# Kernel optimization log

Hardware: AMD Instinct MI355X
Metric: run time of the kernel (lower is better)

## Reference

```python
import jax, jax.numpy as jnp
import numpy as np


def setup_inputs() -> dict:
    key = jax.random.key(0)
    k1, k2, k3, k4 = jax.random.split(key, 4)
    H, D, Dh, NH = 4096, 1024, 256, 4  # height, weight1, INNER_FEATURE_A, heads
    x = jax.random.normal(k1, (H, D), dtype=jnp.float32)
    Wq = jax.random.normal(k2, (NH, D, Dh), dtype=jnp.float32)
    lin_w = jax.random.normal(k3, (D, NH * Dh), dtype=jnp.float32)  # torch Linear weight [out, in]
    lin_b = jax.random.normal(k4, (D,), dtype=jnp.float32)
    return {"x": x, "Wq": Wq, "lin_w": lin_w, "lin_b": lin_b}


def reference(x, Wq, lin_w, lin_b):
    # Faithful to source: Q = K = V = x @ Wq1 (original uses Wq1 for all three).
    # mask_flag=False -> multiplicative all-ones mask (identity, elided).
    # qkv: [heads, H, Dh]
    qkv = jnp.einsum('hd,ndk->nhk', x, Wq)
    # scores: [heads, H, H]; softmax over dim=1 of the 2D matrix = last axis here
    scores = jnp.einsum('nqk,npk->nqp', qkv, qkv)
    attn = jax.nn.softmax(scores, axis=-1)
    z = jnp.einsum('nqp,npk->nqk', attn, qkv)  # [heads, H, Dh]
    # concat heads along feature dim -> [H, heads*Dh]
    zc = jnp.transpose(z, (1, 0, 2)).reshape(x.shape[0], -1)
    return zc @ lin_w.T + lin_b
```

## Files before the change

### kernel.cpp

```cpp
#include <hip/hip_runtime.h>
#include <math.h>

#define SEQ 4096
#define DIM 1024
#define DHEAD 256
#define NHEADS 4

typedef __attribute__((ext_vector_type(8))) short bf16x8;
typedef __attribute__((ext_vector_type(4))) float f32x4;
typedef __attribute__((ext_vector_type(4))) short short4v;
typedef __attribute__((ext_vector_type(8))) short short8v;

__device__ __forceinline__ unsigned short f2b(float f) {
    union { float f; unsigned u; } v; v.f = f;
    unsigned r = v.u + 0x7FFFu + ((v.u >> 16) & 1u);
    return (unsigned short)(r >> 16);
}
__device__ __forceinline__ float b2f(unsigned short u) {
    union { unsigned u; float f; } v; v.u = ((unsigned)u) << 16;
    return v.f;
}

__device__ __forceinline__ void gll16(const void* g, void* lds) {
    __builtin_amdgcn_global_load_lds(
        (const __attribute__((address_space(1))) unsigned*)g,
        (__attribute__((address_space(3))) unsigned*)lds, 16, 0, 0);
}

__device__ __forceinline__ f32x4 mfma16(bf16x8 a, bf16x8 b, f32x4 c) {
    return __builtin_amdgcn_mfma_f32_16x16x32_bf16(a, b, c, 0, 0, 0);
}

__global__ __launch_bounds__(256)
void conv_kernel(const float* __restrict__ in, unsigned short* __restrict__ out, int n4) {
    int i = blockIdx.x * 256 + threadIdx.x;
    if (i >= n4) return;
    float4 v = ((const float4*)in)[i];
    short4v o;
    o[0] = (short)f2b(v.x); o[1] = (short)f2b(v.y);
    o[2] = (short)f2b(v.z); o[3] = (short)f2b(v.w);
    *(short4v*)(out + (size_t)i * 4) = o;
}

__global__ __launch_bounds__(256)
void wqt_kernel(const float* __restrict__ Wq, unsigned short* __restrict__ WqT) {
    __shared__ unsigned short T[64][72];
    const int tid = threadIdx.x;
    const int h = blockIdx.z;
    const int d0 = blockIdx.x * 64, c0 = blockIdx.y * 64;
#pragma unroll
    for (int it = 0; it < 4; ++it) {
        int f = tid + 256 * it;
        int row = f >> 4, cg = f & 15;
        float4 v = *(const float4*)&Wq[((size_t)(h * DIM + d0 + row)) * DHEAD + c0 + cg * 4];
        T[row][cg * 4 + 0] = f2b(v.x); T[row][cg * 4 + 1] = f2b(v.y);
        T[row][cg * 4 + 2] = f2b(v.z); T[row][cg * 4 + 3] = f2b(v.w);
    }
    __syncthreads();
#pragma unroll
    for (int it = 0; it < 2; ++it) {
        int f = tid + 256 * it;
        int cl = f >> 3, dg = f & 7;
        short8v o;
#pragma unroll
        for (int e = 0; e < 8; ++e) o[e] = (short)T[dg * 8 + e][cl];
        *(short8v*)&WqT[((size_t)(h * DHEAD + c0 + cl)) * DIM + d0 + dg * 8] = o;
    }
}

__global__ __launch_bounds__(256)
void qkvt_kernel(const unsigned short* __restrict__ qkv, unsigned short* __restrict__ qkvT) {
    __shared__ unsigned short T[64][72];
    const int tid = threadIdx.x;
    const int h = blockIdx.z;
    const int r0 = blockIdx.x * 64, c0 = blockIdx.y * 64;
#pragma unroll
    for (int it = 0; it < 2; ++it) {
        int f = tid + 256 * it;
        int row = f >> 3, cg = f & 7;
        short8v v = *(const short8v*)&qkv[((size_t)h * SEQ + r0 + row) * DHEAD + c0 + cg * 8];
#pragma unroll
        for (int e = 0; e < 8; ++e) T[row][cg * 8 + e] = (unsigned short)v[e];
    }
    __syncthreads();
#pragma unroll
    for (int it = 0; it < 2; ++it) {
        int f = tid + 256 * it;
        int cl = f >> 3, rg = f & 7;
        short8v o;
#pragma unroll
        for (int e = 0; e < 8; ++e) o[e] = (short)T[rg * 8 + e][cl];
        *(short8v*)&qkvT[((size_t)h * DHEAD + c0 + cl) * SEQ + r0 + rg * 8] = o;
    }
}

__global__ __launch_bounds__(256)
void qkv_gemm_kernel(const unsigned short* __restrict__ A,
                     const unsigned short* __restrict__ B,
                     unsigned short* __restrict__ qkv) {
    __shared__ unsigned short As[128 * 64];
    __shared__ unsigned short Bs[128 * 64];
    const int tid = threadIdx.x, w = tid >> 6, l = tid & 63;
    const int g = l >> 4, r16 = l & 15;
    const int m0 = blockIdx.x * 128, n0 = blockIdx.y * 128;
    const int wm = (w >> 1) * 64, wn = (w & 1) * 64;

    f32x4 acc[4][4];
#pragma unroll
    for (int mr = 0; mr < 4; ++mr)
#pragma unroll
        for (int nr = 0; nr < 4; ++nr) acc[mr][nr] = (f32x4){0.f, 0.f, 0.f, 0.f};

    for (int kb = 0; kb < DIM; kb += 64) {
        __syncthreads();
#pragma unroll
        for (int cc = 0; cc < 4; ++cc) {
            int row = w * 32 + cc * 8 + (l >> 3);
            int c = (l & 7) ^ (row & 7);
            gll16(&A[(size_t)(m0 + row) * DIM + kb + c * 8], &As[(size_t)(w * 32 + cc * 8) * 64]);
            gll16(&B[(size_t)(n0 + row) * DIM + kb + c * 8], &Bs[(size_t)(w * 32 + cc * 8) * 64]);
        }
        __syncthreads();
#pragma unroll
        for (int s = 0; s < 2; ++s) {
            bf16x8 af[4], bf[4];
#pragma unroll
            for (int mr = 0; mr < 4; ++mr) {
                int row = wm + mr * 16 + r16;
                int st = (s * 4 + g) ^ (row & 7);
                af[mr] = *(const bf16x8*)&As[row * 64 + st * 8];
            }
#pragma unroll
            for (int nr = 0; nr < 4; ++nr) {
                int row = wn + nr * 16 + r16;
                int st = (s * 4 + g) ^ (row & 7);
                bf[nr] = *(const bf16x8*)&Bs[row * 64 + st * 8];
            }
#pragma unroll
            for (int mr = 0; mr < 4; ++mr)
#pragma unroll
                for (int nr = 0; nr < 4; ++nr)
                    acc[mr][nr] = mfma16(af[mr], bf[nr], acc[mr][nr]);
        }
    }
#pragma unroll
    for (int mr = 0; mr < 4; ++mr)
#pragma unroll
        for (int nr = 0; nr < 4; ++nr) {
            int n = n0 + wn + nr * 16 + r16;
            int h = n >> 8, c = n & 255;
#pragma unroll
            for (int r = 0; r < 4; ++r) {
                int m = m0 + wm + mr * 16 + g * 4 + r;
                qkv[((size_t)h * SEQ + m) * DHEAD + c] = f2b(acc[mr][nr][r]);
            }
        }
}

__global__ __launch_bounds__(256, 2)
void attn_kernel(const unsigned short* __restrict__ qkv,
                 const unsigned short* __restrict__ qkvT,
                 unsigned short* __restrict__ p0,
                 unsigned short* __restrict__ p1,
                 float* __restrict__ ml) {
    __shared__ unsigned short Ks[64 * 256];
    __shared__ unsigned short Vt[256 * 64];
    __shared__ unsigned short Ps[64 * 64];
    __shared__ float alphaS[64];
    __shared__ float mS[64], lS[64];

    const int tid = threadIdx.x, w = tid >> 6, l = tid & 63;
    const int g = l >> 4, r16 = l & 15;
    const int bid = blockIdx.x;
    const int h = (bid & 7) >> 1, hf = bid & 1;
    const int qb = bid >> 3;
    const unsigned short* __restrict__ qh = qkv + (size_t)h * SEQ * DHEAD;
    const unsigned short* __restrict__ qth = qkvT + (size_t)h * DHEAD * SEQ;
    const int jb0 = hf * (SEQ / 2);
    const int NT = (SEQ / 2) / 64;

    bf16x8 qf[8];
    {
        const unsigned short* qrow = qh + (size_t)(qb * 64 + w * 16 + r16) * DHEAD + g * 8;
#pragma unroll
        for (int s = 0; s < 8; ++s) qf[s] = *(const bf16x8*)(qrow + s * 32);
    }

    f32x4 Oacc[16];
#pragma unroll
    for (int i = 0; i < 16; ++i) Oacc[i] = (f32x4){0.f, 0.f, 0.f, 0.f};
    float mrow = -INFINITY, lrow = 0.f;

    for (int t = 0; t < NT; ++t) {
        const int jb = jb0 + t * 64;
        __syncthreads();
#pragma unroll
        for (int cc = 0; cc < 8; ++cc) {
            int ch = w * 8 + cc;
            int j = ch * 2 + (l >> 5);
            int cp = l & 31;
            int c = (cp & 24) | ((cp & 7) ^ (j & 7));
            gll16(&qh[(size_t)(jb + j) * DHEAD + c * 8], &Ks[(size_t)ch * 512]);
        }
#pragma unroll
        for (int cc = 0; cc < 8; ++cc) {
            int ch = w * 8 + cc;
            int d = ch * 8 + (l >> 3);
            int c = (l & 7) ^ (d & 7);
            gll16(&qth[(size_t)d * SEQ + jb + c * 8], &Vt[(size_t)ch * 512]);
        }
        __syncthreads();

        f32x4 sacc[4];
#pragma unroll
        for (int jt = 0; jt < 4; ++jt) sacc[jt] = (f32x4){0.f, 0.f, 0.f, 0.f};
        __builtin_amdgcn_s_setprio(1);
#pragma unroll
        for (int s = 0; s < 8; ++s)
#pragma unroll
            for (int jt = 0; jt < 4; ++jt) {
                int j = jt * 16 + r16;
                int c = s * 4 + g;
                int st = (c & 24) | ((c & 7) ^ (j & 7));
                bf16x8 af = *(const bf16x8*)&Ks[j * 256 + st * 8];
                sacc[jt] = mfma16(af, qf[s], sacc[jt]);
            }
        __builtin_amdgcn_s_setprio(0);

        float mx = sacc[0][0];
#pragma unroll
        for (int jt = 0; jt < 4; ++jt)
#pragma unroll
            for (int r = 0; r < 4; ++r) mx = fmaxf(mx, sacc[jt][r]);
        mx = fmaxf(mx, __shfl_xor(mx, 16, 64));
        mx = fmaxf(mx, __shfl_xor(mx, 32, 64));

        float mn = fmaxf(mrow, mx);
        float alpha = __expf(mrow - mn);
        mrow = mn;

        float rsum = 0.f;
        short4v pf[4];
#pragma unroll
        for (int jt = 0; jt < 4; ++jt)
#pragma unroll
            for (int r = 0; r < 4; ++r) {
                float p = __expf(sacc[jt][r] - mrow);
                rsum += p;
                pf[jt][r] = (short)f2b(p);
            }
        rsum += __shfl_xor(rsum, 16, 64);
        rsum += __shfl_xor(rsum, 32, 64);
        lrow = lrow * alpha + rsum;

#pragma unroll
        for (int jt = 0; jt < 4; ++jt) {
            int st = (jt * 2 + (g >> 1)) ^ (r16 & 7);
            *(short4v*)&Ps[(w * 16 + r16) * 64 + st * 8 + (g & 1) * 4] = pf[jt];
        }
        if (g == 0) alphaS[w * 16 + r16] = alpha;
        __syncthreads();

        bf16x8 pa[8];
#pragma unroll
        for (int qs = 0; qs < 4; ++qs) {
            f32x4 av = *(const f32x4*)&alphaS[qs * 16 + g * 4];
#pragma unroll
            for (int dt = 0; dt < 4; ++dt)
#pragma unroll
                for (int r = 0; r < 4; ++r) Oacc[qs * 4 + dt][r] *= av[r];
#pragma unroll
            for (int s2 = 0; s2 < 2; ++s2) {
                int qrow = qs * 16 + r16;
                int st = (s2 * 4 + g) ^ (qrow & 7);
                pa[qs * 2 + s2] = *(const bf16x8*)&Ps[qrow * 64 + st * 8];
            }
        }
        __builtin_amdgcn_s_setprio(1);
#pragma unroll
        for (int dt = 0; dt < 4; ++dt) {
            int d = w * 64 + dt * 16 + r16;
#pragma unroll
            for (int s2 = 0; s2 < 2; ++s2) {
                int st = (s2 * 4 + g) ^ (d & 7);
                bf16x8 bv = *(const bf16x8*)&Vt[d * 64 + st * 8];
#pragma unroll
                for (int qs = 0; qs < 4; ++qs)
                    Oacc[qs * 4 + dt] = mfma16(pa[qs * 2 + s2], bv, Oacc[qs * 4 + dt]);
            }
        }
        __builtin_amdgcn_s_setprio(0);
    }

    if (g == 0) { mS[w * 16 + r16] = mrow; lS[w * 16 + r16] = lrow; }
    __syncthreads();
    unsigned short* po = hf ? p1 : p0;
#pragma unroll
    for (int qs = 0; qs < 4; ++qs)
#pragma unroll
        for (int dt = 0; dt < 4; ++dt) {
            int d = w * 64 + dt * 16 + r16;
#pragma unroll
            for (int r = 0; r < 4; ++r) {
                int q = qb * 64 + qs * 16 + g * 4 + r;
                po[(size_t)q * (NHEADS * DHEAD) + h * DHEAD + d] = f2b(Oacc[qs * 4 + dt][r]);
            }
        }
    if (tid < 64) {
        int q = qb * 64 + tid;
        float* mlq = ml + ((size_t)(hf * NHEADS + h) * SEQ + q) * 2;
        mlq[0] = mS[tid]; mlq[1] = lS[tid];
    }
}

__global__ __launch_bounds__(256)
void combine_kernel(const unsigned short* __restrict__ pa,
                    const unsigned short* __restrict__ pb,
                    const float* __restrict__ ml,
                    unsigned short* __restrict__ zc) {
    size_t t = (size_t)blockIdx.x * 256 + threadIdx.x;
    size_t f = t * 8;
    int q = (int)(f >> 10);
    int h = (int)((f >> 8) & 3);
    const float* ml0 = ml + ((size_t)h * SEQ + q) * 2;
    const float* ml1 = ml + ((size_t)(NHEADS + h) * SEQ + q) * 2;
    float m0 = ml0[0], l0 = ml0[1], m1 = ml1[0], l1 = ml1[1];
    float M = fmaxf(m0, m1);
    float e0 = __expf(m0 - M), e1 = __expf(m1 - M);
    float inv = 1.f / (e0 * l0 + e1 * l1);
    e0 *= inv; e1 *= inv;
    short8v a = *(const short8v*)(pa + f);
    short8v b = *(const short8v*)(pb + f);
    short8v o;
#pragma unroll
    for (int e = 0; e < 8; ++e)
        o[e] = (short)f2b(e0 * b2f((unsigned short)a[e]) + e1 * b2f((unsigned short)b[e]));
    *(short8v*)(zc + f) = o;
}

__global__ __launch_bounds__(256)
void out_gemm_kernel(const unsigned short* __restrict__ A,
                     const unsigned short* __restrict__ B,
                     const float* __restrict__ lb, float* __restrict__ out) {
    __shared__ unsigned short As[128 * 64];
    __shared__ unsigned short Bs[128 * 64];
    const int tid = threadIdx.x, w = tid >> 6, l = tid & 63;
    const int g = l >> 4, r16 = l & 15;
    const int m0 = blockIdx.x * 128, n0 = blockIdx.y * 128;
    const int wm = (w >> 1) * 64, wn = (w & 1) * 64;

    f32x4 acc[4][4];
#pragma unroll
    for (int mr = 0; mr < 4; ++mr)
#pragma unroll
        for (int nr = 0; nr < 4; ++nr) acc[mr][nr] = (f32x4){0.f, 0.f, 0.f, 0.f};

    for (int kb = 0; kb < DIM; kb += 64) {
        __syncthreads();
#pragma unroll
        for (int cc = 0; cc < 4; ++cc) {
            int row = w * 32 + cc * 8 + (l >> 3);
            int c = (l & 7) ^ (row & 7);
            gll16(&A[(size_t)(m0 + row) * DIM + kb + c * 8], &As[(size_t)(w * 32 + cc * 8) * 64]);
            gll16(&B[(size_t)(n0 + row) * DIM + kb + c * 8], &Bs[(size_t)(w * 32 + cc * 8) * 64]);
        }
        __syncthreads();
#pragma unroll
        for (int s = 0; s < 2; ++s) {
            bf16x8 af[4], bf[4];
#pragma unroll
            for (int mr = 0; mr < 4; ++mr) {
                int row = wm + mr * 16 + r16;
                int st = (s * 4 + g) ^ (row & 7);
                af[mr] = *(const bf16x8*)&As[row * 64 + st * 8];
            }
#pragma unroll
            for (int nr = 0; nr < 4; ++nr) {
                int row = wn + nr * 16 + r16;
                int st = (s * 4 + g) ^ (row & 7);
                bf[nr] = *(const bf16x8*)&Bs[row * 64 + st * 8];
            }
#pragma unroll
            for (int mr = 0; mr < 4; ++mr)
#pragma unroll
                for (int nr = 0; nr < 4; ++nr)
                    acc[mr][nr] = mfma16(af[mr], bf[nr], acc[mr][nr]);
        }
    }
#pragma unroll
    for (int mr = 0; mr < 4; ++mr)
#pragma unroll
        for (int nr = 0; nr < 4; ++nr) {
            int n = n0 + wn + nr * 16 + r16;
            float bv = lb[n];
#pragma unroll
            for (int r = 0; r < 4; ++r) {
                int m = m0 + wm + mr * 16 + g * 4 + r;
                out[(size_t)m * DIM + n] = acc[mr][nr][r] + bv;
            }
        }
}

extern "C" void kernel_launch(void* const* d_in, const int* in_sizes, int n_in,
                              void* d_out, int out_size, void* d_ws, size_t ws_size,
                              hipStream_t stream) {
    const float* x  = (const float*)d_in[0];
    const float* Wq = (const float*)d_in[1];
    const float* lw = (const float*)d_in[2];
    const float* lb = (const float*)d_in[3];
    float* out = (float*)d_out;

    char* wsb = (char*)d_ws;
    unsigned short* qkvb = (unsigned short*)(wsb);
    unsigned short* qkvT = (unsigned short*)(wsb + ((size_t)8 << 20));
    unsigned short* xb   = (unsigned short*)(wsb + ((size_t)16 << 20));
    unsigned short* p0   = xb;
    unsigned short* WqT  = (unsigned short*)(wsb + ((size_t)24 << 20));
    float*          ml   = (float*)(wsb + ((size_t)24 << 20));
    unsigned short* lwb  = (unsigned short*)(wsb + ((size_t)26 << 20));
    unsigned short* p1   = (unsigned short*)d_out;

    conv_kernel<<<4096, 256, 0, stream>>>(x, xb, (SEQ * DIM) / 4);
    conv_kernel<<<1024, 256, 0, stream>>>(lw, lwb, (DIM * DIM) / 4);
    wqt_kernel<<<dim3(16, 4, 4), 256, 0, stream>>>(Wq, WqT);
    qkv_gemm_kernel<<<dim3(SEQ / 128, DIM / 128), 256, 0, stream>>>(xb, WqT, qkvb);
    qkvt_kernel<<<dim3(64, 4, 4), 256, 0, stream>>>(qkvb, qkvT);
    attn_kernel<<<512, 256, 0, stream>>>(qkvb, qkvT, p0, p1, ml);
    combine_kernel<<<(SEQ * DIM / 8) / 256, 256, 0, stream>>>(p0, p1, ml, p0);
    out_gemm_kernel<<<dim3(SEQ / 128, DIM / 128), 256, 0, stream>>>(p0, lwb, lb, out);
}
```

Before: 165.4 us.

## Fuse transpose into QKV GEMM, double-buffer K, lazy rescale in attention

The QKV GEMM epilogue now also writes the transposed bf16 copy, which removes the separate transpose kernel launch and its extra read and write of QKV. The attention kernel double-buffers the K tile in LDS with async global-to-LDS loads prefetched one tile ahead, and loads V fragments straight from global memory into registers instead of staging them in LDS. It also adds a lazy softmax rescale: the running max only updates when the new max exceeds it by more than 8, and the O rescale is skipped when every alpha is 1. This cuts exp and multiply work, but accepts bf16 probabilities up to e^8 with the matching risk to accuracy, and the transposed stores in the GEMM are narrow 8-byte writes.

```diff
diff --git a/kernel.cpp b/kernel.cpp
--- a/kernel.cpp
+++ b/kernel.cpp
@@ -69,35 +69,10 @@
 }
 
 __global__ __launch_bounds__(256)
-void qkvt_kernel(const unsigned short* __restrict__ qkv, unsigned short* __restrict__ qkvT) {
-    __shared__ unsigned short T[64][72];
-    const int tid = threadIdx.x;
-    const int h = blockIdx.z;
-    const int r0 = blockIdx.x * 64, c0 = blockIdx.y * 64;
-#pragma unroll
-    for (int it = 0; it < 2; ++it) {
-        int f = tid + 256 * it;
-        int row = f >> 3, cg = f & 7;
-        short8v v = *(const short8v*)&qkv[((size_t)h * SEQ + r0 + row) * DHEAD + c0 + cg * 8];
-#pragma unroll
-        for (int e = 0; e < 8; ++e) T[row][cg * 8 + e] = (unsigned short)v[e];
-    }
-    __syncthreads();
-#pragma unroll
-    for (int it = 0; it < 2; ++it) {
-        int f = tid + 256 * it;
-        int cl = f >> 3, rg = f & 7;
-        short8v o;
-#pragma unroll
-        for (int e = 0; e < 8; ++e) o[e] = (short)T[rg * 8 + e][cl];
-        *(short8v*)&qkvT[((size_t)h * DHEAD + c0 + cl) * SEQ + r0 + rg * 8] = o;
-    }
-}
-
-__global__ __launch_bounds__(256)
 void qkv_gemm_kernel(const unsigned short* __restrict__ A,
                      const unsigned short* __restrict__ B,
-                     unsigned short* __restrict__ qkv) {
+                     unsigned short* __restrict__ qkv,
+                     unsigned short* __restrict__ qkvT) {
     __shared__ unsigned short As[128 * 64];
     __shared__ unsigned short Bs[128 * 64];
     const int tid = threadIdx.x, w = tid >> 6, l = tid & 63;
@@ -149,11 +124,15 @@
         for (int nr = 0; nr < 4; ++nr) {
             int n = n0 + wn + nr * 16 + r16;
             int h = n >> 8, c = n & 255;
+            int mb = m0 + wm + mr * 16 + g * 4;
+            short4v tv;
 #pragma unroll
             for (int r = 0; r < 4; ++r) {
-                int m = m0 + wm + mr * 16 + g * 4 + r;
-                qkv[((size_t)h * SEQ + m) * DHEAD + c] = f2b(acc[mr][nr][r]);
-            }
+                unsigned short b = f2b(acc[mr][nr][r]);
+                qkv[((size_t)h * SEQ + mb + r) * DHEAD + c] = b;
+                tv[r] = (short)b;
+            }
+            *(short4v*)&qkvT[((size_t)h * DHEAD + c) * SEQ + mb] = tv;
         }
 }
 
@@ -163,8 +142,7 @@
                  unsigned short* __restrict__ p0,
                  unsigned short* __restrict__ p1,
                  float* __restrict__ ml) {
-    __shared__ unsigned short Ks[64 * 256];
-    __shared__ unsigned short Vt[256 * 64];
+    __shared__ unsigned short Ks[2][64 * 256];
     __shared__ unsigned short Ps[64 * 64];
     __shared__ float alphaS[64];
     __shared__ float mS[64], lS[64];
@@ -186,31 +164,48 @@
         for (int s = 0; s < 8; ++s) qf[s] = *(const bf16x8*)(qrow + s * 32);
     }
 
+#define STAGEK(buf, jb)                                                             \
+    {                                                                               \
+        _Pragma("unroll")                                                           \
+        for (int cc = 0; cc < 8; ++cc) {                                            \
+            int ch = w * 8 + cc;                                                    \
+            int j = ch * 2 + (l >> 5);                                              \
+            int cp = l & 31;                                                        \
+            int c = (cp & 24) | ((cp & 7) ^ (j & 7));                               \
+            gll16(&qh[(size_t)((jb) + j) * DHEAD + c * 8], &Ks[buf][(size_t)ch * 512]); \
+        }                                                                           \
+    }
+
+    STAGEK(0, jb0);
+
     f32x4 Oacc[16];
 #pragma unroll
     for (int i = 0; i < 16; ++i) Oacc[i] = (f32x4){0.f, 0.f, 0.f, 0.f};
     float mrow = -INFINITY, lrow = 0.f;
 
     for (int t = 0; t < NT; ++t) {
+        const int cur = t & 1;
         const int jb = jb0 + t * 64;
-        __syncthreads();
-#pragma unroll
-        for (int cc = 0; cc < 8; ++cc) {
-            int ch = w * 8 + cc;
-            int j = ch * 2 + (l >> 5);
-            int cp = l & 31;
-            int c = (cp & 24) | ((cp & 7) ^ (j & 7));
-            gll16(&qh[(size_t)(jb + j) * DHEAD + c * 8], &Ks[(size_t)ch * 512]);
-        }
-#pragma unroll
-        for (int cc = 0; cc < 8; ++cc) {
-            int ch = w * 8 + cc;
-            int d = ch * 8 + (l >> 3);
-            int c = (l & 7) ^ (d & 7);
-            gll16(&qth[(size_t)d * SEQ + jb + c * 8], &Vt[(size_t)ch * 512]);
-        }
-        __syncthreads();
-
+
+        __builtin_amdgcn_sched_barrier(0);
+        asm volatile("s_waitcnt vmcnt(0)" ::: "memory");
+        __builtin_amdgcn_s_barrier();
+        __builtin_amdgcn_sched_barrier(0);
+
+        bf16x8 bv[4][2];
+#pragma unroll
+        for (int dt = 0; dt < 4; ++dt) {
+            int d = w * 64 + dt * 16 + r16;
+#pragma unroll
+            for (int s2 = 0; s2 < 2; ++s2)
+                bv[dt][s2] = *(const bf16x8*)&qth[(size_t)d * SEQ + jb + s2 * 32 + g * 8];
+        }
+        __builtin_amdgcn_sched_barrier(0);
+
+        if (t + 1 < NT) STAGEK(cur ^ 1, jb0 + (t + 1) * 64);
+        __builtin_amdgcn_sched_barrier(0);
+
+        const unsigned short* Kb = &Ks[cur][0];
         f32x4 sacc[4];
 #pragma unroll
         for (int jt = 0; jt < 4; ++jt) sacc[jt] = (f32x4){0.f, 0.f, 0.f, 0.f};
@@ -222,7 +217,7 @@
                 int j = jt * 16 + r16;
                 int c = s * 4 + g;
                 int st = (c & 24) | ((c & 7) ^ (j & 7));
-                bf16x8 af = *(const bf16x8*)&Ks[j * 256 + st * 8];
+                bf16x8 af = *(const bf16x8*)&Kb[j * 256 + st * 8];
                 sacc[jt] = mfma16(af, qf[s], sacc[jt]);
             }
         __builtin_amdgcn_s_setprio(0);
@@ -235,9 +230,12 @@
         mx = fmaxf(mx, __shfl_xor(mx, 16, 64));
         mx = fmaxf(mx, __shfl_xor(mx, 32, 64));
 
-        float mn = fmaxf(mrow, mx);
-        float alpha = __expf(mrow - mn);
-        mrow = mn;
+        float alpha = 1.f;
+        if (!__all(mx <= mrow + 8.f)) {
+            float mn = fmaxf(mrow, mx);
+            alpha = __expf(mrow - mn);
+            mrow = mn;
+        }
 
         float rsum = 0.f;
         short4v pf[4];
@@ -259,16 +257,22 @@
             *(short4v*)&Ps[(w * 16 + r16) * 64 + st * 8 + (g & 1) * 4] = pf[jt];
         }
         if (g == 0) alphaS[w * 16 + r16] = alpha;
-        __syncthreads();
+
+        __builtin_amdgcn_sched_barrier(0);
+        asm volatile("s_waitcnt lgkmcnt(0)" ::: "memory");
+        __builtin_amdgcn_s_barrier();
+        __builtin_amdgcn_sched_barrier(0);
 
         bf16x8 pa[8];
 #pragma unroll
         for (int qs = 0; qs < 4; ++qs) {
             f32x4 av = *(const f32x4*)&alphaS[qs * 16 + g * 4];
-#pragma unroll
-            for (int dt = 0; dt < 4; ++dt)
-#pragma unroll
-                for (int r = 0; r < 4; ++r) Oacc[qs * 4 + dt][r] *= av[r];
+            if (!__all((av[0] == 1.f) & (av[1] == 1.f) & (av[2] == 1.f) & (av[3] == 1.f))) {
+#pragma unroll
+                for (int dt = 0; dt < 4; ++dt)
+#pragma unroll
+                    for (int r = 0; r < 4; ++r) Oacc[qs * 4 + dt][r] *= av[r];
+            }
 #pragma unroll
             for (int s2 = 0; s2 < 2; ++s2) {
                 int qrow = qs * 16 + r16;
@@ -278,19 +282,17 @@
         }
         __builtin_amdgcn_s_setprio(1);
 #pragma unroll
-        for (int dt = 0; dt < 4; ++dt) {
-            int d = w * 64 + dt * 16 + r16;
-#pragma unroll
-            for (int s2 = 0; s2 < 2; ++s2) {
-                int st = (s2 * 4 + g) ^ (d & 7);
-                bf16x8 bv = *(const bf16x8*)&Vt[d * 64 + st * 8];
+        for (int dt = 0; dt < 4; ++dt)
+#pragma unroll
+            for (int s2 = 0; s2 < 2; ++s2)
 #pragma unroll
                 for (int qs = 0; qs < 4; ++qs)
-                    Oacc[qs * 4 + dt] = mfma16(pa[qs * 2 + s2], bv, Oacc[qs * 4 + dt]);
-            }
-        }
+                    Oacc[qs * 4 + dt] = mfma16(pa[qs * 2 + s2], bv[dt][s2], Oacc[qs * 4 + dt]);
         __builtin_amdgcn_s_setprio(0);
     }
+#undef STAGEK
+
+    asm volatile("s_waitcnt vmcnt(0)" ::: "memory");
 
     if (g == 0) { mS[w * 16 + r16] = mrow; lS[w * 16 + r16] = lrow; }
     __syncthreads();
@@ -423,8 +425,7 @@
     conv_kernel<<<4096, 256, 0, stream>>>(x, xb, (SEQ * DIM) / 4);
     conv_kernel<<<1024, 256, 0, stream>>>(lw, lwb, (DIM * DIM) / 4);
     wqt_kernel<<<dim3(16, 4, 4), 256, 0, stream>>>(Wq, WqT);
-    qkv_gemm_kernel<<<dim3(SEQ / 128, DIM / 128), 256, 0, stream>>>(xb, WqT, qkvb);
-    qkvt_kernel<<<dim3(64, 4, 4), 256, 0, stream>>>(qkvb, qkvT);
+    qkv_gemm_kernel<<<dim3(SEQ / 128, DIM / 128), 256, 0, stream>>>(xb, WqT, qkvb, qkvT);
     attn_kernel<<<512, 256, 0, stream>>>(qkvb, qkvT, p0, p1, ml);
     combine_kernel<<<(SEQ * DIM / 8) / 256, 256, 0, stream>>>(p0, p1, ml, p0);
     out_gemm_kernel<<<dim3(SEQ / 128, DIM / 128), 256, 0, stream>>>(p0, lwb, lb, out);
```

Result: slower. 179.9 us (+8.8%).
